# Performance work log

Hardware: AMD Instinct MI355X
Metric: run time of the kernel (lower is better)

Reference implementation:

```python
import jax, jax.numpy as jnp
import numpy as np

NUM_JOINTS = 24
NUM_GRAPHS = 65536
# SMPL-like humanoid kinematic tree: parent[i] < i, root has parent -1
PARENT_TREE = np.array([-1, 0, 1, 2, 3, 0, 5, 6, 7, 0, 9, 10, 11, 12, 11,
                        14, 15, 16, 11, 18, 19, 20, 12, 22], dtype=np.int64)


def rotation_6d_to_matrix(d6):
    # standard 6D rotation representation -> 3x3 rotation matrix (rows b1,b2,b3)
    a1, a2 = d6[..., :3], d6[..., 3:]
    b1 = a1 / (jnp.linalg.norm(a1, axis=-1, keepdims=True) + 1e-12)
    a2p = a2 - jnp.sum(b1 * a2, axis=-1, keepdims=True) * b1
    b2 = a2p / (jnp.linalg.norm(a2p, axis=-1, keepdims=True) + 1e-12)
    b3 = jnp.cross(b1, b2)
    return jnp.stack([b1, b2, b3], axis=-2)  # [..., 3, 3]


def setup_inputs() -> dict:
    key = jax.random.key(0)
    k1, k2 = jax.random.split(key)
    B, N = NUM_GRAPHS, NUM_JOINTS
    x = jax.random.normal(k1, (B * N, 6), dtype=jnp.float32)
    offset = jax.random.normal(k2, (B * N, 3), dtype=jnp.float32)
    parent = jnp.tile(jnp.asarray(PARENT_TREE), B)  # [B*N], valid tree per graph
    return {"x": x, "parent": parent, "offset": offset, "num_graphs": B}


def reference(x, parent, offset, num_graphs):
    B = num_graphs
    x = x.reshape(B, -1, x.shape[-1])            # [B, N, 6]
    N = x.shape[1]
    offset = offset.reshape(B, N, 3)             # [B, N, 3]
    parent_np = np.asarray(parent).reshape(B, -1)[0]  # static tree structure

    T = rotation_6d_to_matrix(x)                 # [B, N, 3, 3] local rotations

    pos = [None] * N   # world positions per joint, each [B, 3]
    rot = [None] * N   # world rotations per joint, each [B, 3, 3]
    for i in range(N):  # N is small/static; parent-before-child order
        p = int(parent_np[i])
        if p == -1:
            pos[i] = jnp.zeros((B, 3), dtype=x.dtype)
            rot[i] = T[:, i]
        else:
            pos[i] = jnp.einsum('bij,bj->bi', rot[p], offset[:, i]) + pos[p]
            rot[i] = jnp.einsum('bij,bjk->bik', rot[p], T[:, i])

    positions = jnp.stack(pos, axis=1)           # [B, N, 3]
    return positions.reshape(-1, 3)              # [B*N, 3]
```

## Files before the change

kernel.cpp:

```cpp
#include <hip/hip_runtime.h>
#include <math.h>


#define PAD 65
#define G   64

#define XS(f,g)   arena[(f)*PAD + (g)]
#define OS(f,g)   arena[(144+(f))*PAD + (g)]
#define OUTS(r,g) arena[(144+(r))*PAD + (g)]
#define HF(r,g)   arena[(216+(r))*PAD + (g)]

__device__ __forceinline__ void rot6d(const float a[6], float T[9]) {
    float n1 = sqrtf(a[0]*a[0] + a[1]*a[1] + a[2]*a[2]) + 1e-12f;
    float i1 = 1.0f / n1;
    float b1x = a[0]*i1, b1y = a[1]*i1, b1z = a[2]*i1;
    float d = b1x*a[3] + b1y*a[4] + b1z*a[5];
    float ax = a[3] - d*b1x, ay = a[4] - d*b1y, az = a[5] - d*b1z;
    float n2 = sqrtf(ax*ax + ay*ay + az*az) + 1e-12f;
    float i2 = 1.0f / n2;
    float b2x = ax*i2, b2y = ay*i2, b2z = az*i2;
    T[0] = b1x; T[1] = b1y; T[2] = b1z;
    T[3] = b2x; T[4] = b2y; T[5] = b2z;
    T[6] = b1y*b2z - b1z*b2y;
    T[7] = b1z*b2x - b1x*b2z;
    T[8] = b1x*b2y - b1y*b2x;
}

template<int J>
__device__ __forceinline__ void pullX(const float* arena, int t, float T[9]) {
    float a[6];
#pragma unroll
    for (int c = 0; c < 6; ++c) a[c] = XS(6*J+c, t);
    rot6d(a, T);
}

template<int J>
__device__ __forceinline__ void pull(const float* arena, int t, float T[9], float o[3]) {
    float a[6];
#pragma unroll
    for (int c = 0; c < 6; ++c) a[c] = XS(6*J+c, t);
#pragma unroll
    for (int c = 0; c < 3; ++c) o[c] = OS(3*J+c, t);
    rot6d(a, T);
}

template<int J>
__device__ __forceinline__ void chain_step(float* arena, int t, float R[9], float P[3],
                                           const float T[9], const float o[3]) {
    float p0 = R[0]*o[0] + R[1]*o[1] + R[2]*o[2] + P[0];
    float p1 = R[3]*o[0] + R[4]*o[1] + R[5]*o[2] + P[1];
    float p2 = R[6]*o[0] + R[7]*o[1] + R[8]*o[2] + P[2];
    float Rn[9];
#pragma unroll
    for (int i = 0; i < 3; ++i)
#pragma unroll
        for (int k = 0; k < 3; ++k)
            Rn[i*3+k] = R[i*3+0]*T[0+k] + R[i*3+1]*T[3+k] + R[i*3+2]*T[6+k];
#pragma unroll
    for (int i = 0; i < 9; ++i) R[i] = Rn[i];
    P[0] = p0; P[1] = p1; P[2] = p2;
    OUTS(3*J+0, t) = p0; OUTS(3*J+1, t) = p1; OUTS(3*J+2, t) = p2;
}

__global__ __launch_bounds__(256, 2) void fk_kernel(const float* __restrict__ x,
                                                    const float* __restrict__ off,
                                                    float* __restrict__ out) {
    __shared__ float arena[240 * PAD];
    const int tid = threadIdx.x;
    const int w = tid >> 6;
    const int t = tid & 63;
    const long gb0 = (long)blockIdx.x * G;
    const float4* x4 = (const float4*)x;
    const float2* o2 = (const float2*)off;

    float4 xr[9]; float2 orr[9];
#pragma unroll
    for (int k = 0; k < 9; ++k) xr[k]  = x4[gb0*36 + k*256 + tid];
#pragma unroll
    for (int k = 0; k < 9; ++k) orr[k] = o2[gb0*36 + k*256 + tid];
#pragma unroll
    for (int k = 0; k < 9; ++k) {
        int i = k*256 + tid; int g = i/36, e = i - g*36;
        XS(4*e+0, g) = xr[k].x; XS(4*e+1, g) = xr[k].y;
        XS(4*e+2, g) = xr[k].z; XS(4*e+3, g) = xr[k].w;
    }
#pragma unroll
    for (int k = 0; k < 9; ++k) {
        int i = k*256 + tid; int g = i/36, e = i - g*36;
        OS(2*e+0, g) = orr[k].x; OS(2*e+1, g) = orr[k].y;
    }
    __syncthreads();

    float Ta[8][9], oa[8][3];
    float R[9], P[3];

    if (w == 0) {
        pullX<0>(arena, t, R);
        pull<1>(arena, t, Ta[0], oa[0]);
        pull<2>(arena, t, Ta[1], oa[1]);
        pull<3>(arena, t, Ta[2], oa[2]);
        pull<4>(arena, t, Ta[3], oa[3]);
        pull<22>(arena, t, Ta[4], oa[4]);
        pull<23>(arena, t, Ta[5], oa[5]);
        P[0] = P[1] = P[2] = 0.0f;
        OUTS(0, t) = 0.0f; OUTS(1, t) = 0.0f; OUTS(2, t) = 0.0f;
        chain_step<1>(arena, t, R, P, Ta[0], oa[0]);
        chain_step<2>(arena, t, R, P, Ta[1], oa[1]);
        chain_step<3>(arena, t, R, P, Ta[2], oa[2]);
        chain_step<4>(arena, t, R, P, Ta[3], oa[3]);
    } else if (w == 1) {
        pullX<0>(arena, t, R);
        pull<5>(arena, t, Ta[0], oa[0]);
        pull<6>(arena, t, Ta[1], oa[1]);
        pull<7>(arena, t, Ta[2], oa[2]);
        pull<8>(arena, t, Ta[3], oa[3]);
        P[0] = P[1] = P[2] = 0.0f;
        chain_step<5>(arena, t, R, P, Ta[0], oa[0]);
        chain_step<6>(arena, t, R, P, Ta[1], oa[1]);
        chain_step<7>(arena, t, R, P, Ta[2], oa[2]);
        chain_step<8>(arena, t, R, P, Ta[3], oa[3]);
    } else if (w == 2) {
        pullX<0>(arena, t, R);
        pull<9> (arena, t, Ta[0], oa[0]);
        pull<10>(arena, t, Ta[1], oa[1]);
        pull<11>(arena, t, Ta[2], oa[2]);
        pull<12>(arena, t, Ta[3], oa[3]);
        pull<13>(arena, t, Ta[4], oa[4]);
        P[0] = P[1] = P[2] = 0.0f;
        chain_step<9> (arena, t, R, P, Ta[0], oa[0]);
        chain_step<10>(arena, t, R, P, Ta[1], oa[1]);
        chain_step<11>(arena, t, R, P, Ta[2], oa[2]);
#pragma unroll
        for (int i = 0; i < 9; ++i) HF(i, t) = R[i];
#pragma unroll
        for (int c = 0; c < 3; ++c) HF(9+c, t) = P[c];
        chain_step<12>(arena, t, R, P, Ta[3], oa[3]);
#pragma unroll
        for (int i = 0; i < 9; ++i) HF(12+i, t) = R[i];
#pragma unroll
        for (int c = 0; c < 3; ++c) HF(21+c, t) = P[c];
        chain_step<13>(arena, t, R, P, Ta[4], oa[4]);
    } else {
        pull<14>(arena, t, Ta[0], oa[0]);
        pull<15>(arena, t, Ta[1], oa[1]);
        pull<16>(arena, t, Ta[2], oa[2]);
        pull<17>(arena, t, Ta[3], oa[3]);
        pull<18>(arena, t, Ta[4], oa[4]);
        pull<19>(arena, t, Ta[5], oa[5]);
        pull<20>(arena, t, Ta[6], oa[6]);
        pull<21>(arena, t, Ta[7], oa[7]);
    }
    __syncthreads();

    if (w == 0) {
#pragma unroll
        for (int i = 0; i < 9; ++i) R[i] = HF(12+i, t);
#pragma unroll
        for (int c = 0; c < 3; ++c) P[c] = HF(21+c, t);
        chain_step<22>(arena, t, R, P, Ta[4], oa[4]);
        chain_step<23>(arena, t, R, P, Ta[5], oa[5]);
    } else if (w == 3) {
#pragma unroll
        for (int i = 0; i < 9; ++i) R[i] = HF(i, t);
#pragma unroll
        for (int c = 0; c < 3; ++c) P[c] = HF(9+c, t);
        chain_step<14>(arena, t, R, P, Ta[0], oa[0]);
        chain_step<15>(arena, t, R, P, Ta[1], oa[1]);
        chain_step<16>(arena, t, R, P, Ta[2], oa[2]);
        chain_step<17>(arena, t, R, P, Ta[3], oa[3]);
#pragma unroll
        for (int i = 0; i < 9; ++i) R[i] = HF(i, t);
#pragma unroll
        for (int c = 0; c < 3; ++c) P[c] = HF(9+c, t);
        chain_step<18>(arena, t, R, P, Ta[4], oa[4]);
        chain_step<19>(arena, t, R, P, Ta[5], oa[5]);
        chain_step<20>(arena, t, R, P, Ta[6], oa[6]);
        chain_step<21>(arena, t, R, P, Ta[7], oa[7]);
    }
    __syncthreads();

    float4* out4 = (float4*)out;
#pragma unroll
    for (int k = 0; k < 5; ++k) {
        int i = k*256 + tid;
        if (i < 1152) {
            int g = i/18, e = i - g*18;
            float4 v;
            v.x = OUTS(4*e+0, g); v.y = OUTS(4*e+1, g);
            v.z = OUTS(4*e+2, g); v.w = OUTS(4*e+3, g);
            out4[gb0*18 + i] = v;
        }
    }
}

__global__ __launch_bounds__(256) void fk_tail(const float* __restrict__ x,
                                               const float* __restrict__ off,
                                               float* __restrict__ out,
                                               int b0, int B) {
    int b = b0 + blockIdx.x * blockDim.x + threadIdx.x;
    if (b >= B) return;
    const float* xb = x + (size_t)b * 144;
    const float* ob = off + (size_t)b * 72;
    float* P = out + (size_t)b * 72;
    float R[9], Pc[3], R0[9], R11[9], P11[3], R12[9], P12[3];
    {
        float a[6] = {xb[0],xb[1],xb[2],xb[3],xb[4],xb[5]};
        rot6d(a, R);
        Pc[0] = Pc[1] = Pc[2] = 0.0f;
        P[0] = P[1] = P[2] = 0.0f;
        for (int i = 0; i < 9; ++i) R0[i] = R[i];
    }
    for (int j = 1; j < 24; ++j) {
        float Rp[9], Pp[3];
        if (j==1||j==5||j==9) { for (int i=0;i<9;++i) Rp[i]=R0[i]; Pp[0]=Pp[1]=Pp[2]=0.f; }
        else if (j==14||j==18) { for (int i=0;i<9;++i) Rp[i]=R11[i]; Pp[0]=P11[0];Pp[1]=P11[1];Pp[2]=P11[2]; }
        else if (j==22)   { for (int i=0;i<9;++i) Rp[i]=R12[i]; Pp[0]=P12[0];Pp[1]=P12[1];Pp[2]=P12[2]; }
        else              { for (int i=0;i<9;++i) Rp[i]=R[i];   Pp[0]=Pc[0];Pp[1]=Pc[1];Pp[2]=Pc[2]; }
        float T[9];
        float a[6] = {xb[j*6+0],xb[j*6+1],xb[j*6+2],xb[j*6+3],xb[j*6+4],xb[j*6+5]};
        rot6d(a, T);
        float o0=ob[j*3+0],o1=ob[j*3+1],o2=ob[j*3+2];
        Pc[0]=Rp[0]*o0+Rp[1]*o1+Rp[2]*o2+Pp[0];
        Pc[1]=Rp[3]*o0+Rp[4]*o1+Rp[5]*o2+Pp[1];
        Pc[2]=Rp[6]*o0+Rp[7]*o1+Rp[8]*o2+Pp[2];
        for (int i=0;i<3;++i) for (int k=0;k<3;++k) {
            float s=0.f; for (int m=0;m<3;++m) s+=Rp[i*3+m]*T[m*3+k];
            R[i*3+k]=s;
        }
        P[j*3+0]=Pc[0]; P[j*3+1]=Pc[1]; P[j*3+2]=Pc[2];
        if (j==11) { for (int i=0;i<9;++i) R11[i]=R[i]; P11[0]=Pc[0];P11[1]=Pc[1];P11[2]=Pc[2]; }
        if (j==12) { for (int i=0;i<9;++i) R12[i]=R[i]; P12[0]=Pc[0];P12[1]=Pc[1];P12[2]=Pc[2]; }
    }
}

extern "C" void kernel_launch(void* const* d_in, const int* in_sizes, int n_in,
                              void* d_out, int out_size, void* d_ws, size_t ws_size,
                              hipStream_t stream) {
    const float* x   = (const float*)d_in[0];
    const float* off = (const float*)d_in[2];
    float* out = (float*)d_out;
    int B = in_sizes[0] / 144;
    int nb = B / G;
    if (nb > 0)
        fk_kernel<<<nb, 256, 0, stream>>>(x, off, out);
    int rem = B - nb * G;
    if (rem > 0)
        fk_tail<<<(rem + 255) / 256, 256, 0, stream>>>(x, off, out, nb * G, B);
}
```

Before: 21.56 us.

## Process two tiles per block, prefetching the second tile's inputs into registers

Each block now handles two 64-graph tiles instead of one, halving the grid. After staging the first tile into LDS, the block issues global loads for the second tile into registers, so those loads overlap the first tile's compute and output flush. Costs are more live registers (the prefetched loads stay resident during compute) and extra barriers, plus fewer blocks to spread across CUs.

```diff
diff --git a/kernel.cpp b/kernel.cpp
--- a/kernel.cpp
+++ b/kernel.cpp
@@ -62,22 +62,19 @@
     OUTS(3*J+0, t) = p0; OUTS(3*J+1, t) = p1; OUTS(3*J+2, t) = p2;
 }
 
-__global__ __launch_bounds__(256, 2) void fk_kernel(const float* __restrict__ x,
-                                                    const float* __restrict__ off,
-                                                    float* __restrict__ out) {
-    __shared__ float arena[240 * PAD];
-    const int tid = threadIdx.x;
-    const int w = tid >> 6;
-    const int t = tid & 63;
-    const long gb0 = (long)blockIdx.x * G;
-    const float4* x4 = (const float4*)x;
-    const float2* o2 = (const float2*)off;
-
-    float4 xr[9]; float2 orr[9];
+__device__ __forceinline__ void load_regs(const float4* __restrict__ x4,
+                                          const float2* __restrict__ o2,
+                                          long tile, int tid,
+                                          float4 xr[9], float2 orr[9]) {
+    long gb0 = tile * G;
 #pragma unroll
     for (int k = 0; k < 9; ++k) xr[k]  = x4[gb0*36 + k*256 + tid];
 #pragma unroll
     for (int k = 0; k < 9; ++k) orr[k] = o2[gb0*36 + k*256 + tid];
+}
+
+__device__ __forceinline__ void stage_lds(float* arena, int tid,
+                                          const float4 xr[9], const float2 orr[9]) {
 #pragma unroll
     for (int k = 0; k < 9; ++k) {
         int i = k*256 + tid; int g = i/36, e = i - g*36;
@@ -89,11 +86,11 @@
         int i = k*256 + tid; int g = i/36, e = i - g*36;
         OS(2*e+0, g) = orr[k].x; OS(2*e+1, g) = orr[k].y;
     }
-    __syncthreads();
-
+}
+
+__device__ __forceinline__ void compute_tile(float* arena, int w, int t) {
     float Ta[8][9], oa[8][3];
     float R[9], P[3];
-
     if (w == 0) {
         pullX<0>(arena, t, R);
         pull<1>(arena, t, Ta[0], oa[0]);
@@ -151,7 +148,6 @@
         pull<21>(arena, t, Ta[7], oa[7]);
     }
     __syncthreads();
-
     if (w == 0) {
 #pragma unroll
         for (int i = 0; i < 9; ++i) R[i] = HF(12+i, t);
@@ -177,9 +173,11 @@
         chain_step<20>(arena, t, R, P, Ta[6], oa[6]);
         chain_step<21>(arena, t, R, P, Ta[7], oa[7]);
     }
-    __syncthreads();
-
-    float4* out4 = (float4*)out;
+}
+
+__device__ __forceinline__ void flush_tile(const float* arena, float4* __restrict__ out4,
+                                           long tile, int tid) {
+    long gb0 = tile * G;
 #pragma unroll
     for (int k = 0; k < 5; ++k) {
         int i = k*256 + tid;
@@ -190,6 +188,43 @@
             v.z = OUTS(4*e+2, g); v.w = OUTS(4*e+3, g);
             out4[gb0*18 + i] = v;
         }
+    }
+}
+
+__global__ __launch_bounds__(256, 2) void fk_kernel(const float* __restrict__ x,
+                                                    const float* __restrict__ off,
+                                                    float* __restrict__ out,
+                                                    int ntiles) {
+    __shared__ float arena[240 * PAD];
+    const int tid = threadIdx.x;
+    const int w = tid >> 6;
+    const int t = tid & 63;
+    const float4* x4 = (const float4*)x;
+    const float2* o2 = (const float2*)off;
+    float4* out4 = (float4*)out;
+
+    long tile0 = (long)blockIdx.x * 2;
+    long tile1 = tile0 + 1;
+    bool has2 = (tile1 < ntiles);
+
+    float4 xr[9]; float2 orr[9];
+
+    load_regs(x4, o2, tile0, tid, xr, orr);
+    stage_lds(arena, tid, xr, orr);
+    if (has2) load_regs(x4, o2, tile1, tid, xr, orr);
+    __syncthreads();
+
+    compute_tile(arena, w, t);
+    __syncthreads();
+    flush_tile(arena, out4, tile0, tid);
+
+    if (has2) {
+        __syncthreads();
+        stage_lds(arena, tid, xr, orr);
+        __syncthreads();
+        compute_tile(arena, w, t);
+        __syncthreads();
+        flush_tile(arena, out4, tile1, tid);
     }
 }
 
@@ -240,10 +275,11 @@
     const float* off = (const float*)d_in[2];
     float* out = (float*)d_out;
     int B = in_sizes[0] / 144;
-    int nb = B / G;
-    if (nb > 0)
-        fk_kernel<<<nb, 256, 0, stream>>>(x, off, out);
-    int rem = B - nb * G;
+    int ntiles = B / G;
+    int nblk = (ntiles + 1) / 2;
+    if (nblk > 0)
+        fk_kernel<<<nblk, 256, 0, stream>>>(x, off, out, ntiles);
+    int rem = B - ntiles * G;
     if (rem > 0)
-        fk_tail<<<(rem + 255) / 256, 256, 0, stream>>>(x, off, out, nb * G, B);
-}
+        fk_tail<<<(rem + 255) / 256, 256, 0, stream>>>(x, off, out, ntiles * G, B);
+}
```

Measured after the change: 23.61 us. 9.5% more time.
